# Kernel optimization log

Measured on AMD Instinct MI355X. Metric: run time of the kernel, lower is better.

## Reference

```python
import jax, jax.numpy as jnp
import numpy as np

B, F = 1024, 784
OUT, OR_T, AND_T = 1024, 32, 16
IDX_RANGE = 1 + 2 * F  # column 0 is the constant-true column


def setup_inputs() -> dict:
    key = jax.random.key(0)
    kx, kw = jax.random.split(key)
    # Binary inputs (0/1) stored as float32; module calls x.bool() i.e. x != 0.
    x = jax.random.randint(kx, (B, F), 0, 2).astype(jnp.float32)
    # Integer gate wiring: indices into [const_true | x | ~x].
    weights = jax.random.randint(kw, (OUT, OR_T, AND_T), 0, IDX_RANGE).astype(jnp.int32)
    return {"x": x, "weights": weights}


def reference(x, weights):
    out_f, or_t, and_t = weights.shape
    b = x.shape[0]
    xb = x != 0                                            # [B, F] bool
    ones = jnp.ones((b, 1), dtype=bool)
    x_in = jnp.concatenate([ones, xb, ~xb], axis=1)        # [B, 1+2F]
    # or_padding_mask: an OR-term is active unless all its AND indices are 0
    or_mask = ~jnp.all(weights == 0, axis=-1)              # [OUT, OR_T]
    # Gather selected booleans, then AND over and_terms, OR over or_terms
    x_sel = x_in[:, weights.reshape(-1)]                   # [B, OUT*OR_T*AND_T]
    x_bin = x_sel.reshape(b, out_f, or_t, and_t)
    x_and = jnp.all(x_bin, axis=-1) & or_mask              # [B, OUT, OR_T]
    x_or = jnp.any(x_and, axis=-1)                         # [B, OUT]
    return x_or
```

## Files before the change

### kernel.cpp

```cpp
#include <hip/hip_runtime.h>
#include <stdint.h>

#define BATCH 1024
#define FEAT  784
#define OUTF  1024
#define OR_T  32
#define AND_T 16
#define NIDX  1569
#define LWORDS 1600

typedef unsigned long long u64;

__global__ __launch_bounds__(1024) void binlayer(const float* __restrict__ x,
                                                 const int* __restrict__ w,
                                                 int* __restrict__ out) {
    __shared__ u64 lbits[LWORDS];
    __shared__ u64 red[1024];

    const int g    = blockIdx.x;
    const int ob   = blockIdx.y;
    const int tid  = threadIdx.x;
    const int lane = tid & 63;
    const int wv   = tid >> 6;

    const int start = wv * 12 + (wv < 4 ? wv : 4);
    const int cnt   = (wv < 4) ? 13 : 12;
    const float4* xrow = (const float4*)(x + (size_t)(g * 64 + lane) * FEAT);
    for (int i = 0; i < cnt; ++i) {
        const int f4 = start + i;
        const float4 v = xrow[f4];
        const int f = f4 * 4;
        const u64 m0 = __ballot(v.x != 0.0f);
        const u64 m1 = __ballot(v.y != 0.0f);
        const u64 m2 = __ballot(v.z != 0.0f);
        const u64 m3 = __ballot(v.w != 0.0f);
        const u64 mv = (lane == 0) ? m0 : (lane == 1) ? m1 : (lane == 2) ? m2 : m3;
        if (lane < 4) {
            lbits[1 + f + lane]   = mv;
            lbits[785 + f + lane] = ~mv;
        }
    }
    if (tid == 0) lbits[0] = ~0ull;
    __syncthreads();

    const int o_local = tid & 63;
    const int tg      = tid >> 6;
    const int o       = ob * 64 + o_local;

    const int4* wq = (const int4*)(w + ((size_t)o * OR_T + tg * 2) * AND_T);

    u64 orv = 0;
    #pragma unroll
    for (int tt = 0; tt < 2; ++tt) {
        u64 a = ~0ull;
        int zor = 0;
        #pragma unroll
        for (int k = 0; k < 4; ++k) {
            const int4 wi = wq[tt * 4 + k];
            zor |= wi.x | wi.y | wi.z | wi.w;
            a &= lbits[wi.x];
            a &= lbits[wi.y];
            a &= lbits[wi.z];
            a &= lbits[wi.w];
        }
        if (zor != 0) orv |= a;
    }

    red[tid] = orv;
    __syncthreads();

    u64 full = 0;
    #pragma unroll
    for (int j = 0; j < 16; ++j) full |= red[o_local + j * 64];

    int* outg = out + (size_t)(g * 64) * OUTF + (size_t)ob * 64;
    #pragma unroll
    for (int jj = 0; jj < 4; ++jj) {
        const int j = tg * 4 + jj;
        outg[(size_t)j * OUTF + o_local] = (int)((full >> j) & 1);
    }
}

extern "C" void kernel_launch(void* const* d_in, const int* in_sizes, int n_in,
                              void* d_out, int out_size, void* d_ws, size_t ws_size,
                              hipStream_t stream) {
    const float* x = (const float*)d_in[0];
    const int*   w = (const int*)d_in[1];
    int* out = (int*)d_out;

    binlayer<<<dim3(BATCH / 64, OUTF / 64), 1024, 0, stream>>>(x, w, out);
}
```

Baseline: 75.34 us.

## Process 128 batch rows per block with paired 64-bit bitplanes

Each block now packs two 64-row batch halves into a u64x2 shared bit table, so every weight-index gather serves 128 batch rows instead of 64. Output tiles shrink to 32 outputs with one OR-term per thread, and OR-reduction across half-waves uses a shuffle before a padded shared-memory reduction. This halves the number of weight reads and LDS lookups per batch row, but adds more x-loading work per block and 16-byte LDS gathers that may conflict more.

```diff
diff --git a/kernel.cpp b/kernel.cpp
--- a/kernel.cpp
+++ b/kernel.cpp
@@ -7,15 +7,22 @@
 #define OR_T  32
 #define AND_T 16
 #define NIDX  1569
-#define LWORDS 1600
 
 typedef unsigned long long u64;
+typedef __attribute__((ext_vector_type(2))) u64 u64x2;
+
+static __device__ __forceinline__ u64 or_shfl_xor32(u64 v) {
+    unsigned int lo = __shfl_xor((unsigned int)v, 32);
+    unsigned int hi = __shfl_xor((unsigned int)(v >> 32), 32);
+    return v | (((u64)hi << 32) | (u64)lo);
+}
 
 __global__ __launch_bounds__(1024) void binlayer(const float* __restrict__ x,
                                                  const int* __restrict__ w,
                                                  int* __restrict__ out) {
-    __shared__ u64 lbits[LWORDS];
-    __shared__ u64 red[1024];
+    __shared__ u64x2 lbits[1600];
+    __shared__ u64 red_lo[16 * 33];
+    __shared__ u64 red_hi[16 * 33];
 
     const int g    = blockIdx.x;
     const int ob   = blockIdx.y;
@@ -23,9 +30,13 @@
     const int lane = tid & 63;
     const int wv   = tid >> 6;
 
-    const int start = wv * 12 + (wv < 4 ? wv : 4);
-    const int cnt   = (wv < 4) ? 13 : 12;
-    const float4* xrow = (const float4*)(x + (size_t)(g * 64 + lane) * FEAT);
+    const int half = wv >> 3;
+    const int wsub = wv & 7;
+    const int cnt   = (wsub < 4) ? 25 : 24;
+    const int start = wsub * 24 + (wsub < 4 ? wsub : 4);
+    const float4* xrow =
+        (const float4*)(x + (size_t)(g * 128 + half * 64 + lane) * FEAT);
+
     for (int i = 0; i < cnt; ++i) {
         const int f4 = start + i;
         const float4 v = xrow[f4];
@@ -36,48 +47,60 @@
         const u64 m3 = __ballot(v.w != 0.0f);
         const u64 mv = (lane == 0) ? m0 : (lane == 1) ? m1 : (lane == 2) ? m2 : m3;
         if (lane < 4) {
-            lbits[1 + f + lane]   = mv;
-            lbits[785 + f + lane] = ~mv;
+            if (half == 0) {
+                lbits[1 + f + lane].x   = mv;
+                lbits[785 + f + lane].x = ~mv;
+            } else {
+                lbits[1 + f + lane].y   = mv;
+                lbits[785 + f + lane].y = ~mv;
+            }
         }
     }
-    if (tid == 0) lbits[0] = ~0ull;
+    if (tid == 0) { lbits[0].x = ~0ull; lbits[0].y = ~0ull; }
     __syncthreads();
 
-    const int o_local = tid & 63;
-    const int tg      = tid >> 6;
-    const int o       = ob * 64 + o_local;
+    const int o_local = tid & 31;
+    const int tg      = tid >> 5;
+    const int o       = ob * 32 + o_local;
 
-    const int4* wq = (const int4*)(w + ((size_t)o * OR_T + tg * 2) * AND_T);
+    const int4* wq = (const int4*)(w + ((size_t)o * OR_T + tg) * AND_T);
 
-    u64 orv = 0;
+    u64x2 a = {~0ull, ~0ull};
+    int zor = 0;
     #pragma unroll
-    for (int tt = 0; tt < 2; ++tt) {
-        u64 a = ~0ull;
-        int zor = 0;
-        #pragma unroll
-        for (int k = 0; k < 4; ++k) {
-            const int4 wi = wq[tt * 4 + k];
-            zor |= wi.x | wi.y | wi.z | wi.w;
-            a &= lbits[wi.x];
-            a &= lbits[wi.y];
-            a &= lbits[wi.z];
-            a &= lbits[wi.w];
-        }
-        if (zor != 0) orv |= a;
+    for (int k = 0; k < 4; ++k) {
+        const int4 wi = wq[k];
+        zor |= wi.x | wi.y | wi.z | wi.w;
+        a &= lbits[wi.x];
+        a &= lbits[wi.y];
+        a &= lbits[wi.z];
+        a &= lbits[wi.w];
     }
+    u64 vlo = (zor != 0) ? a.x : 0ull;
+    u64 vhi = (zor != 0) ? a.y : 0ull;
 
-    red[tid] = orv;
+    vlo = or_shfl_xor32(vlo);
+    vhi = or_shfl_xor32(vhi);
+    if (lane < 32) {
+        red_lo[wv * 33 + o_local] = vlo;
+        red_hi[wv * 33 + o_local] = vhi;
+    }
     __syncthreads();
 
-    u64 full = 0;
+    const int o2   = tid & 31;
+    const int rgrp = tid >> 5;
+    const int j    = rgrp >> 4;
+    const u64* plane = j ? red_hi : red_lo;
+
+    u64 v = 0;
     #pragma unroll
-    for (int j = 0; j < 16; ++j) full |= red[o_local + j * 64];
+    for (int k = 0; k < 16; ++k) v |= plane[k * 33 + o2];
 
-    int* outg = out + (size_t)(g * 64) * OUTF + (size_t)ob * 64;
+    const int rb = (rgrp & 15) * 4;
+    int* outp = out + (size_t)(g * 128 + j * 64 + rb) * OUTF + ob * 32 + o2;
     #pragma unroll
-    for (int jj = 0; jj < 4; ++jj) {
-        const int j = tg * 4 + jj;
-        outg[(size_t)j * OUTF + o_local] = (int)((full >> j) & 1);
+    for (int i = 0; i < 4; ++i) {
+        outp[(size_t)i * OUTF] = (int)((v >> (rb + i)) & 1);
     }
 }
 
@@ -88,5 +111,5 @@
     const int*   w = (const int*)d_in[1];
     int* out = (int*)d_out;
 
-    binlayer<<<dim3(BATCH / 64, OUTF / 64), 1024, 0, stream>>>(x, w, out);
+    binlayer<<<dim3(BATCH / 128, OUTF / 32), 1024, 0, stream>>>(x, w, out);
 }
```

After: 88.05 us. 16.9% more time.
